# Kernel tuning notes

Measured on AMD Instinct MI355X. Metric: run time of the kernel, lower is better.

The kernel has to match this reference:

```python
import jax, jax.numpy as jnp
import numpy as np

HEADS = 8
NEG_SLOPE = 0.2  # PyG GATConv default negative_slope


def segment_softmax(logits, seg, num_segments):
    # logits: [E, H], seg: [E] destination ids
    m = jax.ops.segment_max(logits, seg, num_segments=num_segments)
    m = jnp.where(jnp.isfinite(m), m, 0.0)
    e = jnp.exp(logits - jax.lax.stop_gradient(m)[seg])
    s = jax.ops.segment_sum(e, seg, num_segments=num_segments)
    return e / (s[seg] + 1e-16)


def setup_inputs() -> dict:
    key = jax.random.key(0)
    k1, k2, k3, k4, k5, k6 = jax.random.split(key, 6)
    N, F_IN, H, C, E = 50000, 116, HEADS, 32, 800000
    x = jax.random.normal(k1, (N, F_IN), dtype=jnp.float32)
    edge_index = jax.random.randint(k2, (2, E), 0, N, dtype=jnp.int64)
    # Params (glorot-ish scale)
    W = jax.random.normal(k3, (F_IN, H * C), dtype=jnp.float32) * (1.0 / np.sqrt(F_IN))
    att_src = jax.random.normal(k4, (1, H, C), dtype=jnp.float32) * (1.0 / np.sqrt(C))
    att_dst = jax.random.normal(k5, (1, H, C), dtype=jnp.float32) * (1.0 / np.sqrt(C))
    bias = jnp.zeros((C,), dtype=jnp.float32)
    return {"x": x, "edge_index": edge_index, "W": W, "att_src": att_src, "att_dst": att_dst, "bias": bias}


def reference(x, edge_index, W, att_src, att_dst, bias):
    N = x.shape[0]
    H = HEADS
    C = W.shape[1] // H
    # Shared linear transform: [N, H, C]
    xt = (x @ W).reshape(N, H, C)
    alpha_src = jnp.sum(xt * att_src, axis=-1)  # [N, H]
    alpha_dst = jnp.sum(xt * att_dst, axis=-1)  # [N, H]
    # add_self_loops=True (PyG GATConv default)
    loops = jnp.arange(N, dtype=edge_index.dtype)
    src = jnp.concatenate([edge_index[0], loops])
    dst = jnp.concatenate([edge_index[1], loops])
    # Edge-wise attention logits + segment softmax over destination
    alpha = jax.nn.leaky_relu(alpha_src[src] + alpha_dst[dst], negative_slope=NEG_SLOPE)  # [E', H]
    alpha = segment_softmax(alpha, dst, N)
    # Weighted message aggregation
    msg = xt[src] * alpha[:, :, None]  # [E', H, C]
    out = jax.ops.segment_sum(msg, dst, num_segments=N)  # [N, H, C]
    # concat=False -> mean over heads, then bias
    out = out.mean(axis=1) + bias  # [N, C]
    return jax.nn.relu(out)
```

## Files before the change

kernel.cpp:

```cpp
#include <hip/hip_runtime.h>
#include <hip/hip_bf16.h>


#define F_IN 116
#define HC 256
#define NHEAD 8
#define CDIM 32
#define KP 128
#define ROWS_PB 48
#define DSLOT 64
#define ECHUNK 4096

typedef unsigned int uint32;
typedef short short8 __attribute__((ext_vector_type(8)));
typedef float f32x4 __attribute__((ext_vector_type(4)));

__device__ __forceinline__ unsigned short f2bf(float f) {
    uint32 u = __float_as_uint(f);
    u = (u + 0x7FFF + ((u >> 16) & 1)) >> 16;
    return (unsigned short)u;
}

__global__ void init_k(const float* __restrict__ W,
                       const float* __restrict__ att_s,
                       const float* __restrict__ att_d,
                       unsigned short* __restrict__ WbT,
                       unsigned short* __restrict__ WaT) {
    int idx = blockIdx.x * 256 + threadIdx.x;
    if (idx < 32768) {
        int n = idx >> 7, k = idx & 127;
        WbT[idx] = (k < F_IN) ? f2bf(W[k * HC + n]) : (unsigned short)0;
    } else {
        int aid = idx - 32768;
        int col = aid >> 7, k = aid & 127;
        int tile = col >> 4;
        int cc = col & 15;
        int h = cc & 7, part = cc >> 3;
        const float* att = tile ? att_d : att_s;
        float s = 0.f;
        if (k < F_IN) {
            for (int c = 0; c < CDIM; ++c)
                s = fmaf(W[k * HC + h * CDIM + c], att[h * CDIM + c], s);
        }
        unsigned short hi = f2bf(s);
        unsigned short v = hi;
        if (part) {
            float rem = s - __uint_as_float((uint32)hi << 16);
            v = f2bf(rem);
        }
        WaT[col * KP + k] = v;
    }
}

__global__ __launch_bounds__(256) void scatter_k(const int* __restrict__ src,
                                                 const int* __restrict__ dst,
                                                 int* __restrict__ cnt,
                                                 unsigned short* __restrict__ csr,
                                                 int N, int E) {
    const int t = threadIdx.x;
    const int slice = blockIdx.x & 7;
    const int chunk = blockIdx.x >> 3;
    const int SLICE = (N + 7) >> 3;
    const int lo = slice * SLICE;
    const int hi = (lo + SLICE < N) ? lo + SLICE : N;
    const int ebase = chunk * ECHUNK + t * 4;
#pragma unroll
    for (int it = 0; it < ECHUNK / 1024; ++it) {
        int e = ebase + it * 1024;
        if (e < E) {
            int4 d4 = *(const int4*)&dst[e];
            int4 s4 = *(const int4*)&src[e];
            if (d4.x >= lo && d4.x < hi) {
                int r = atomicAdd(&cnt[d4.x], 1);
                if (r < DSLOT) csr[(d4.x << 6) + r] = (unsigned short)s4.x;
            }
            if (d4.y >= lo && d4.y < hi) {
                int r = atomicAdd(&cnt[d4.y], 1);
                if (r < DSLOT) csr[(d4.y << 6) + r] = (unsigned short)s4.y;
            }
            if (d4.z >= lo && d4.z < hi) {
                int r = atomicAdd(&cnt[d4.z], 1);
                if (r < DSLOT) csr[(d4.z << 6) + r] = (unsigned short)s4.z;
            }
            if (d4.w >= lo && d4.w < hi) {
                int r = atomicAdd(&cnt[d4.w], 1);
                if (r < DSLOT) csr[(d4.w << 6) + r] = (unsigned short)s4.w;
            }
        }
    }
}

__global__ __launch_bounds__(256) void gemm_k(const float* __restrict__ x,
                                              const unsigned short* __restrict__ WbT,
                                              const unsigned short* __restrict__ WaT,
                                              unsigned short* __restrict__ xth,
                                              float* __restrict__ asrc,
                                              float* __restrict__ adst,
                                              int N) {
    const int t = threadIdx.x;
    __shared__ unsigned short xbs[16 * ROWS_PB * 8];
    const int row0 = blockIdx.x * ROWS_PB;
    for (int u = t; u < 16 * ROWS_PB; u += 256) {
        const int g = u / ROWS_PB, r = u - g * ROWS_PB;
        const int gr = row0 + r;
        f32x4 v0 = {0.f, 0.f, 0.f, 0.f}, v1 = {0.f, 0.f, 0.f, 0.f};
        if (gr < N) {
            const f32x4* xp = (const f32x4*)(x + (size_t)gr * F_IN + g * 8);
            if (g < 14) { v0 = xp[0]; v1 = xp[1]; }
            else if (g == 14) { v0 = xp[0]; }
        }
        short8 pk;
        pk[0] = (short)f2bf(v0.x); pk[1] = (short)f2bf(v0.y);
        pk[2] = (short)f2bf(v0.z); pk[3] = (short)f2bf(v0.w);
        pk[4] = (short)f2bf(v1.x); pk[5] = (short)f2bf(v1.y);
        pk[6] = (short)f2bf(v1.z); pk[7] = (short)f2bf(v1.w);
        *(short8*)&xbs[u * 8] = pk;
    }
    __syncthreads();

    const int w = t >> 6, l = t & 63;
    const int q = l >> 4, m = l & 15;
    const int ncol0 = w * 64;

    short8 bfr[4][4];
#pragma unroll
    for (int nt = 0; nt < 4; ++nt)
#pragma unroll
        for (int ks = 0; ks < 4; ++ks)
            bfr[nt][ks] = *(const short8*)&WbT[(size_t)(ncol0 + nt * 16 + m) * KP + ks * 32 + q * 8];

    short8 wa[4];
    if (w < 2) {
#pragma unroll
        for (int ks = 0; ks < 4; ++ks)
            wa[ks] = *(const short8*)&WaT[(size_t)(w * 16 + m) * KP + ks * 32 + q * 8];
    }

    f32x4 acc[3][4];
#pragma unroll
    for (int rt = 0; rt < 3; ++rt)
#pragma unroll
        for (int nt = 0; nt < 4; ++nt) acc[rt][nt] = f32x4{0.f, 0.f, 0.f, 0.f};
    f32x4 acc_a[3];
#pragma unroll
    for (int rt = 0; rt < 3; ++rt) acc_a[rt] = f32x4{0.f, 0.f, 0.f, 0.f};

#pragma unroll
    for (int ks = 0; ks < 4; ++ks) {
        short8 a[3];
#pragma unroll
        for (int rt = 0; rt < 3; ++rt)
            a[rt] = *(const short8*)&xbs[((ks * 4 + q) * ROWS_PB + rt * 16 + m) * 8];
#pragma unroll
        for (int nt = 0; nt < 4; ++nt)
#pragma unroll
            for (int rt = 0; rt < 3; ++rt)
                acc[rt][nt] = __builtin_amdgcn_mfma_f32_16x16x32_bf16(bfr[nt][ks], a[rt], acc[rt][nt], 0, 0, 0);
        if (w < 2) {
#pragma unroll
            for (int rt = 0; rt < 3; ++rt)
                acc_a[rt] = __builtin_amdgcn_mfma_f32_16x16x32_bf16(wa[ks], a[rt], acc_a[rt], 0, 0, 0);
        }
    }

#pragma unroll
    for (int rt = 0; rt < 3; ++rt) {
        const int row = row0 + rt * 16 + m;
        if (row < N) {
#pragma unroll
            for (int nt = 0; nt < 4; ++nt) {
                uint2 pk;
                pk.x = (uint32)f2bf(acc[rt][nt][0]) | ((uint32)f2bf(acc[rt][nt][1]) << 16);
                pk.y = (uint32)f2bf(acc[rt][nt][2]) | ((uint32)f2bf(acc[rt][nt][3]) << 16);
                *(uint2*)&xth[(size_t)row * HC + ncol0 + nt * 16 + q * 4] = pk;
            }
        }
    }

    if (w < 2) {
        float* ap = (w == 0) ? asrc : adst;
#pragma unroll
        for (int rt = 0; rt < 3; ++rt) {
            f32x4 s;
#pragma unroll
            for (int r = 0; r < 4; ++r) {
                float v = acc_a[rt][r];
                s[r] = v + __shfl_xor(v, 32, 64);
            }
            const int row = row0 + rt * 16 + m;
            if (q < 2 && row < N)
                *(f32x4*)&ap[row * NHEAD + q * 4] = s;
        }
    }
}

__global__ __launch_bounds__(256) void aggregate_k(const unsigned short* __restrict__ xth,
                                                   const float* __restrict__ asrc,
                                                   const float* __restrict__ adst,
                                                   const int* __restrict__ cnt,
                                                   const unsigned short* __restrict__ csr,
                                                   const float* __restrict__ bias,
                                                   float* __restrict__ out, int N) {
    const int t = threadIdx.x;
    const int l = t & 63;
    const int n = blockIdx.x * 4 + (t >> 6);
    if (n >= N) return;

    const int h_f = l >> 3;
    const int h_w = l & 7;
    const int e_w = l >> 3;

    const int beg = n << 6;
    int d = cnt[n];
    if (d > DSLOT) d = DSLOT;

    const float adst_hw = adst[n * NHEAD + h_w];

    float zs = asrc[n * NHEAD + h_f] + adst[n * NHEAD + h_f];
    zs = (zs > 0.f) ? zs : 0.2f * zs;
    const float wself = __expf(zs);

    uint2 sv = ((const uint2*)(xth + (size_t)n * HC))[l];
    float a0 = wself * __uint_as_float(sv.x << 16);
    float a1 = wself * __uint_as_float(sv.x & 0xFFFF0000u);
    float a2 = wself * __uint_as_float(sv.y << 16);
    float a3 = wself * __uint_as_float(sv.y & 0xFFFF0000u);
    float wsum = wself;

    const int nfull = d >> 3;
    const int rem = d & 7;
    int pos = beg;
    for (int cch = 0; cch < nfull; ++cch, pos += 8) {
        int s_w = (int)csr[pos + e_w];
        float z = asrc[s_w * NHEAD + h_w] + adst_hw;
        z = (z > 0.f) ? z : 0.2f * z;
        float w_reg = __expf(z);
#pragma unroll
        for (int e = 0; e < 8; ++e) {
            int s = __shfl(s_w, e << 3, 64);
            float w = __shfl(w_reg, (e << 3) + h_f, 64);
            uint2 v = ((const uint2*)(xth + (size_t)s * HC))[l];
            a0 = fmaf(w, __uint_as_float(v.x << 16), a0);
            a1 = fmaf(w, __uint_as_float(v.x & 0xFFFF0000u), a1);
            a2 = fmaf(w, __uint_as_float(v.y << 16), a2);
            a3 = fmaf(w, __uint_as_float(v.y & 0xFFFF0000u), a3);
            wsum += w;
        }
    }
    if (rem) {
        int s_w = (e_w < rem) ? (int)csr[pos + e_w] : n;
        float z = asrc[s_w * NHEAD + h_w] + adst_hw;
        z = (z > 0.f) ? z : 0.2f * z;
        float w_reg = __expf(z);
        for (int e = 0; e < rem; ++e) {
            int s = __shfl(s_w, e << 3, 64);
            float w = __shfl(w_reg, (e << 3) + h_f, 64);
            uint2 v = ((const uint2*)(xth + (size_t)s * HC))[l];
            a0 = fmaf(w, __uint_as_float(v.x << 16), a0);
            a1 = fmaf(w, __uint_as_float(v.x & 0xFFFF0000u), a1);
            a2 = fmaf(w, __uint_as_float(v.y << 16), a2);
            a3 = fmaf(w, __uint_as_float(v.y & 0xFFFF0000u), a3);
            wsum += w;
        }
    }

    const float inv = 1.f / (wsum + 1e-16f);
    a0 *= inv; a1 *= inv; a2 *= inv; a3 *= inv;

#pragma unroll
    for (int o = 8; o <= 32; o <<= 1) {
        a0 += __shfl_xor(a0, o, 64);
        a1 += __shfl_xor(a1, o, 64);
        a2 += __shfl_xor(a2, o, 64);
        a3 += __shfl_xor(a3, o, 64);
    }

    if (l < 8) {
        const float* bp = bias + 4 * l;
        float4 r;
        r.x = fmaxf(a0 * 0.125f + bp[0], 0.f);
        r.y = fmaxf(a1 * 0.125f + bp[1], 0.f);
        r.z = fmaxf(a2 * 0.125f + bp[2], 0.f);
        r.w = fmaxf(a3 * 0.125f + bp[3], 0.f);
        *(float4*)&out[(size_t)n * CDIM + 4 * l] = r;
    }
}

extern "C" void kernel_launch(void* const* d_in, const int* in_sizes, int n_in,
                              void* d_out, int out_size, void* d_ws, size_t ws_size,
                              hipStream_t stream) {
    const float* x     = (const float*)d_in[0];
    const int*   ei    = (const int*)d_in[1];
    const float* W     = (const float*)d_in[2];
    const float* att_s = (const float*)d_in[3];
    const float* att_d = (const float*)d_in[4];
    const float* bias  = (const float*)d_in[5];
    float* out = (float*)d_out;

    const int N = in_sizes[0] / F_IN;
    const int E = in_sizes[1] / 2;

    unsigned short* xth = (unsigned short*)d_ws;
    unsigned short* WbT = xth + (size_t)N * HC;
    float* asrc = (float*)(WbT + 256 * KP);
    float* adst = asrc + (size_t)N * NHEAD;
    int*   cnt  = (int*)(adst + (size_t)N * NHEAD);
    unsigned short* csr = (unsigned short*)(cnt + N);
    unsigned short* WaT = csr + (size_t)N * DSLOT;

    const int Ggemm = (N + ROWS_PB - 1) / ROWS_PB;
    const int nchunk = (E + ECHUNK - 1) / ECHUNK;
    const int Gscat = nchunk * 8;

    (void)hipMemsetAsync(cnt, 0, (size_t)N * sizeof(int), stream);
    init_k<<<144, 256, 0, stream>>>(W, att_s, att_d, WbT, WaT);
    scatter_k<<<Gscat, 256, 0, stream>>>(ei, ei + E, cnt, csr, N, E);
    gemm_k<<<Ggemm, 256, 0, stream>>>(x, WbT, WaT, xth, asrc, adst, N);
    aggregate_k<<<(N + 3) / 4, 256, 0, stream>>>(xth, asrc, adst, cnt, csr, bias, out, N);
}
```

Before: 211.7 us.

## Process each node with half a wavefront using 16-byte bf16 gathers

The aggregation kernel now gives each destination node 32 lanes instead of a full 64-lane wavefront, so one wavefront handles two nodes. Each lane gathers 8 bf16 channels with a single 16-byte load instead of 4 channels with 8 bytes. Edge batches shrink from 8 to 4 per shuffle round, and the cross-head reduction uses xor offsets 4, 8 and 16. The goal is fewer instructions per gathered row and more memory requests in flight, at the cost of twice the accumulator registers per lane.

```diff
diff --git a/kernel.cpp b/kernel.cpp
--- a/kernel.cpp
+++ b/kernel.cpp
@@ -202,13 +202,14 @@
                                                    const float* __restrict__ bias,
                                                    float* __restrict__ out, int N) {
     const int t = threadIdx.x;
-    const int l = t & 63;
-    const int n = blockIdx.x * 4 + (t >> 6);
+    const int lg = t & 31;
+    const int base = t & 32;
+    const int n = blockIdx.x * 8 + (t >> 5);
     if (n >= N) return;
 
-    const int h_f = l >> 3;
-    const int h_w = l & 7;
-    const int e_w = l >> 3;
+    const int h_f = lg >> 2;
+    const int h_w = lg & 7;
+    const int e_w = lg >> 3;
 
     const int beg = n << 6;
     int d = cnt[n];
@@ -220,30 +221,38 @@
     zs = (zs > 0.f) ? zs : 0.2f * zs;
     const float wself = __expf(zs);
 
-    uint2 sv = ((const uint2*)(xth + (size_t)n * HC))[l];
+    uint4 sv = ((const uint4*)(xth + (size_t)n * HC))[lg];
     float a0 = wself * __uint_as_float(sv.x << 16);
     float a1 = wself * __uint_as_float(sv.x & 0xFFFF0000u);
     float a2 = wself * __uint_as_float(sv.y << 16);
     float a3 = wself * __uint_as_float(sv.y & 0xFFFF0000u);
+    float a4 = wself * __uint_as_float(sv.z << 16);
+    float a5 = wself * __uint_as_float(sv.z & 0xFFFF0000u);
+    float a6 = wself * __uint_as_float(sv.w << 16);
+    float a7 = wself * __uint_as_float(sv.w & 0xFFFF0000u);
     float wsum = wself;
 
-    const int nfull = d >> 3;
-    const int rem = d & 7;
+    const int nfull = d >> 2;
+    const int rem = d & 3;
     int pos = beg;
-    for (int cch = 0; cch < nfull; ++cch, pos += 8) {
+    for (int cch = 0; cch < nfull; ++cch, pos += 4) {
         int s_w = (int)csr[pos + e_w];
         float z = asrc[s_w * NHEAD + h_w] + adst_hw;
         z = (z > 0.f) ? z : 0.2f * z;
         float w_reg = __expf(z);
 #pragma unroll
-        for (int e = 0; e < 8; ++e) {
-            int s = __shfl(s_w, e << 3, 64);
-            float w = __shfl(w_reg, (e << 3) + h_f, 64);
-            uint2 v = ((const uint2*)(xth + (size_t)s * HC))[l];
+        for (int e = 0; e < 4; ++e) {
+            int s = __shfl(s_w, base + (e << 3), 64);
+            float w = __shfl(w_reg, base + (e << 3) + h_f, 64);
+            uint4 v = ((const uint4*)(xth + (size_t)s * HC))[lg];
             a0 = fmaf(w, __uint_as_float(v.x << 16), a0);
             a1 = fmaf(w, __uint_as_float(v.x & 0xFFFF0000u), a1);
             a2 = fmaf(w, __uint_as_float(v.y << 16), a2);
             a3 = fmaf(w, __uint_as_float(v.y & 0xFFFF0000u), a3);
+            a4 = fmaf(w, __uint_as_float(v.z << 16), a4);
+            a5 = fmaf(w, __uint_as_float(v.z & 0xFFFF0000u), a5);
+            a6 = fmaf(w, __uint_as_float(v.w << 16), a6);
+            a7 = fmaf(w, __uint_as_float(v.w & 0xFFFF0000u), a7);
             wsum += w;
         }
     }
@@ -253,36 +262,50 @@
         z = (z > 0.f) ? z : 0.2f * z;
         float w_reg = __expf(z);
         for (int e = 0; e < rem; ++e) {
-            int s = __shfl(s_w, e << 3, 64);
-            float w = __shfl(w_reg, (e << 3) + h_f, 64);
-            uint2 v = ((const uint2*)(xth + (size_t)s * HC))[l];
+            int s = __shfl(s_w, base + (e << 3), 64);
+            float w = __shfl(w_reg, base + (e << 3) + h_f, 64);
+            uint4 v = ((const uint4*)(xth + (size_t)s * HC))[lg];
             a0 = fmaf(w, __uint_as_float(v.x << 16), a0);
             a1 = fmaf(w, __uint_as_float(v.x & 0xFFFF0000u), a1);
             a2 = fmaf(w, __uint_as_float(v.y << 16), a2);
             a3 = fmaf(w, __uint_as_float(v.y & 0xFFFF0000u), a3);
+            a4 = fmaf(w, __uint_as_float(v.z << 16), a4);
+            a5 = fmaf(w, __uint_as_float(v.z & 0xFFFF0000u), a5);
+            a6 = fmaf(w, __uint_as_float(v.w << 16), a6);
+            a7 = fmaf(w, __uint_as_float(v.w & 0xFFFF0000u), a7);
             wsum += w;
         }
     }
 
     const float inv = 1.f / (wsum + 1e-16f);
     a0 *= inv; a1 *= inv; a2 *= inv; a3 *= inv;
-
-#pragma unroll
-    for (int o = 8; o <= 32; o <<= 1) {
+    a4 *= inv; a5 *= inv; a6 *= inv; a7 *= inv;
+
+#pragma unroll
+    for (int o = 4; o <= 16; o <<= 1) {
         a0 += __shfl_xor(a0, o, 64);
         a1 += __shfl_xor(a1, o, 64);
         a2 += __shfl_xor(a2, o, 64);
         a3 += __shfl_xor(a3, o, 64);
-    }
-
-    if (l < 8) {
-        const float* bp = bias + 4 * l;
-        float4 r;
-        r.x = fmaxf(a0 * 0.125f + bp[0], 0.f);
-        r.y = fmaxf(a1 * 0.125f + bp[1], 0.f);
-        r.z = fmaxf(a2 * 0.125f + bp[2], 0.f);
-        r.w = fmaxf(a3 * 0.125f + bp[3], 0.f);
-        *(float4*)&out[(size_t)n * CDIM + 4 * l] = r;
+        a4 += __shfl_xor(a4, o, 64);
+        a5 += __shfl_xor(a5, o, 64);
+        a6 += __shfl_xor(a6, o, 64);
+        a7 += __shfl_xor(a7, o, 64);
+    }
+
+    if (lg < 4) {
+        const float* bp = bias + 8 * lg;
+        float4 r0, r1;
+        r0.x = fmaxf(a0 * 0.125f + bp[0], 0.f);
+        r0.y = fmaxf(a1 * 0.125f + bp[1], 0.f);
+        r0.z = fmaxf(a2 * 0.125f + bp[2], 0.f);
+        r0.w = fmaxf(a3 * 0.125f + bp[3], 0.f);
+        r1.x = fmaxf(a4 * 0.125f + bp[4], 0.f);
+        r1.y = fmaxf(a5 * 0.125f + bp[5], 0.f);
+        r1.z = fmaxf(a6 * 0.125f + bp[6], 0.f);
+        r1.w = fmaxf(a7 * 0.125f + bp[7], 0.f);
+        *(float4*)&out[(size_t)n * CDIM + 8 * lg] = r0;
+        *(float4*)&out[(size_t)n * CDIM + 8 * lg + 4] = r1;
     }
 }
 
@@ -316,5 +339,5 @@
     init_k<<<144, 256, 0, stream>>>(W, att_s, att_d, WbT, WaT);
     scatter_k<<<Gscat, 256, 0, stream>>>(ei, ei + E, cnt, csr, N, E);
     gemm_k<<<Ggemm, 256, 0, stream>>>(x, WbT, WaT, xth, asrc, adst, N);
-    aggregate_k<<<(N + 3) / 4, 256, 0, stream>>>(xth, asrc, adst, cnt, csr, bias, out, N);
-}
+    aggregate_k<<<(N + 7) / 8, 256, 0, stream>>>(xth, asrc, adst, cnt, csr, bias, out, N);
+}
```

Measured after the change: 209.9 us. About the same (-0.8%).
